# Kernel optimization log

Measured on AMD Instinct MI355X. Metric: run time of the kernel, lower is better.

The kernel has to match this reference:

```python
import jax, jax.numpy as jnp
import numpy as np

CH, G, K, STRIDE, RR = 256, 16, 7, 1, 4
GROUP = CH // G            # channels per group
PAD = (K - 1) // 2
BN_EPS = 1e-5


def setup_inputs() -> dict:
    key = jax.random.key(0)
    ks = jax.random.split(key, 9)
    b, dim = 16, 4096
    hid = CH // RR  # 64
    return {
        "x": jax.random.normal(ks[0], (b, CH, dim), jnp.float32),
        "w1": jax.random.normal(ks[1], (hid, CH), jnp.float32) * (1.0 / np.sqrt(CH)),
        "b1": jax.random.normal(ks[2], (hid,), jnp.float32) * 0.02,
        "bn_gamma": 1.0 + 0.1 * jax.random.normal(ks[3], (hid,), jnp.float32),
        "bn_beta": 0.1 * jax.random.normal(ks[4], (hid,), jnp.float32),
        "bn_mean": 0.1 * jax.random.normal(ks[5], (hid,), jnp.float32),
        "bn_var": jax.random.uniform(ks[6], (hid,), jnp.float32) + 0.5,
        "w2": jax.random.normal(ks[7], (K * G, hid), jnp.float32) * (1.0 / np.sqrt(hid)),
        "b2": jax.random.normal(ks[8], (K * G,), jnp.float32) * 0.02,
    }


def _involution(x, w1, b1, bn_gamma, bn_beta, bn_mean, bn_var, w2, b2):
    b, ch, dim = x.shape
    L = dim // STRIDE  # out_dim
    # unfold: pad then gather K shifted strided views -> [b, ch, K, L]
    xp = jnp.pad(x, ((0, 0), (0, 0), (PAD, PAD)))
    unfolded = jnp.stack(
        [xp[:, :, k : k + STRIDE * (L - 1) + 1 : STRIDE] for k in range(K)], axis=2
    )
    unfolded = unfolded.reshape(b, G, GROUP, K, L)
    # adaptive max pool to L (windows of size STRIDE); identity when STRIDE == 1
    pooled = x.reshape(b, ch, L, STRIDE).max(axis=-1)
    # kernel generator: 1x1 conv -> relu -> batchnorm (inference) -> 1x1 conv
    h = jnp.einsum("oc,bcl->bol", w1, pooled) + b1[:, None]
    h = jax.nn.relu(h)
    h = (h - bn_mean[:, None]) * jax.lax.rsqrt(bn_var[:, None] + BN_EPS)
    h = h * bn_gamma[:, None] + bn_beta[:, None]
    kern = jnp.einsum("oc,bcl->bol", w2, h) + b2[:, None]  # [b, K*G, L]
    kern = kern.reshape(b, G, K, L)
    # per-location dynamic kernel multiply + reduce over K
    out = jnp.einsum("bgkl,bgckl->bgcl", kern, unfolded)
    return out.reshape(b, ch, L)


def reference(x, w1, b1, bn_gamma, bn_beta, bn_mean, bn_var, w2, b2):
    return _involution(x, w1, b1, bn_gamma, bn_beta, bn_mean, bn_var, w2, b2)
```

## Files before the change

kernel.cpp:

```cpp
#include <hip/hip_runtime.h>

#define BB   16
#define CHN  256
#define DIMN 4096
#define KK   7
#define PADK 3
#define HID  64
#define KGN  112
#define TLC  64
#define NPAN 8
#define PCH  32
#define XSTD 33
#define HSTH 70
#define KSTD 66
#define BN_EPS 1e-5f

typedef __fp16 half2_t __attribute__((ext_vector_type(2)));
typedef __fp16 half8   __attribute__((ext_vector_type(8)));
typedef float  f32x4   __attribute__((ext_vector_type(4)));

union U32H2 { unsigned int u; half2_t h; };

static __device__ __forceinline__ unsigned int packf(float a, float b) {
    U32H2 t; t.h = __builtin_amdgcn_cvt_pkrtz(a, b); return t.u;
}
static __device__ __forceinline__ half2_t ash2(unsigned int u) { U32H2 t; t.u = u; return t.h; }
static __device__ __forceinline__ __fp16 u16h(unsigned short u) {
    return __builtin_bit_cast(__fp16, u);
}
static __device__ __forceinline__ unsigned short hu16(__fp16 h) {
    return __builtin_bit_cast(unsigned short, h);
}

__global__ __launch_bounds__(256) void setup_k(
    const float* __restrict__ w1, const float* __restrict__ w2,
    const float* __restrict__ bn_gamma, const float* __restrict__ bn_beta,
    const float* __restrict__ bn_mean,  const float* __restrict__ bn_var,
    __fp16* __restrict__ w1f, __fp16* __restrict__ w2f,
    float* __restrict__ scb, float* __restrict__ shb) {
    int t = blockIdx.x * 256 + threadIdx.x;
    if (t < HID * CHN) w1f[t] = (__fp16)w1[t];
    if (t < KGN * HID) w2f[t] = (__fp16)w2[t];
    if (t < HID) {
        float s = bn_gamma[t] * rsqrtf(bn_var[t] + BN_EPS);
        scb[t] = s;
        shb[t] = bn_beta[t] - bn_mean[t] * s;
    }
}

template <int OFF>
static __device__ __forceinline__ void extract_kv(const uint4 q[4], float kv[KK][4]) {
#pragma unroll
    for (int k = 0; k < KK; ++k) {
        const int kk = k + OFF;
        const int i  = kk >> 1;
        const int h  = kk & 1;
#pragma unroll
        for (int j = 0; j < 4; ++j) {
            unsigned int u = (&q[i].x)[j];
            half2_t hh = ash2(u);
            kv[k][j] = h ? (float)hh[1] : (float)hh[0];
        }
    }
}

__global__ __launch_bounds__(256, 4) void fused_k(
    const float* __restrict__ x,
    const __fp16* __restrict__ w1f,
    const float* __restrict__ b1,
    const float* __restrict__ scb, const float* __restrict__ shb,
    const __fp16* __restrict__ w2f,
    const float* __restrict__ b2,
    float* __restrict__ out) {
    __shared__ unsigned int   xs[2][PCH * XSTD];
    __shared__ unsigned short hs[HID * HSTH];
    __shared__ unsigned int   ks[56 * KSTD];

    const int t    = threadIdx.x;
    const int lane = t & 63;
    const int w    = t >> 6;
    const int lr   = t & 15;
    const int lg   = (t >> 4) & 3;
    const int b    = blockIdx.x >> 6;
    const int l0   = (blockIdx.x & 63) * TLC;
    const int colL = 16 * w + lr;

    const unsigned short* xs16[2] = {
        (const unsigned short*)xs[0], (const unsigned short*)xs[1] };

    const int colq = t & 15;
    const int chl  = t >> 4;
    const float* xg = x + ((size_t)b * CHN + chl) * DIMN + l0 + 4 * colq;

    float4 pre[2];
#pragma unroll
    for (int i = 0; i < 2; ++i)
        pre[i] = *(const float4*)(xg + (size_t)(16 * i) * DIMN);
#pragma unroll
    for (int i = 0; i < 2; ++i) {
        uint2 v;
        v.x = packf(pre[i].x, pre[i].y);
        v.y = packf(pre[i].z, pre[i].w);
        *(uint2*)&xs[0][(chl + 16 * i) * XSTD + 2 * colq] = v;
    }
    __syncthreads();

    f32x4 acc[4];
#pragma unroll
    for (int of = 0; of < 4; ++of) acc[of] = (f32x4){0.f, 0.f, 0.f, 0.f};

    for (int p = 0; p < NPAN; ++p) {
        if (p + 1 < NPAN) {
#pragma unroll
            for (int i = 0; i < 2; ++i)
                pre[i] = *(const float4*)(xg + (size_t)(32 * (p + 1) + 16 * i) * DIMN);
        }
        const unsigned short* xb = xs16[p & 1];
        half8 bf;
#pragma unroll
        for (int j = 0; j < 8; ++j)
            bf[j] = u16h(xb[(8 * lg + j) * (2 * XSTD) + colL]);
#pragma unroll
        for (int of = 0; of < 4; ++of) {
            half8 af = *(const half8*)(w1f + (16 * of + lr) * CHN + PCH * p + 8 * lg);
            acc[of] = __builtin_amdgcn_mfma_f32_16x16x32_f16(af, bf, acc[of], 0, 0, 0);
        }
        if (p + 1 < NPAN) {
            __syncthreads();
#pragma unroll
            for (int i = 0; i < 2; ++i) {
                uint2 v;
                v.x = packf(pre[i].x, pre[i].y);
                v.y = packf(pre[i].z, pre[i].w);
                *(uint2*)&xs[(p + 1) & 1][(chl + 16 * i) * XSTD + 2 * colq] = v;
            }
            __syncthreads();
        }
    }

#pragma unroll
    for (int of = 0; of < 4; ++of) {
#pragma unroll
        for (int r = 0; r < 4; ++r) {
            const int o = 16 * of + 4 * lg + r;
            float hv = fmaxf(acc[of][r] + b1[o], 0.f) * scb[o] + shb[o];
            hs[o * HSTH + colL] = hu16((__fp16)hv);
        }
    }

    f32x4 acc2[7];
#pragma unroll
    for (int rf = 0; rf < 7; ++rf) acc2[rf] = (f32x4){0.f, 0.f, 0.f, 0.f};

#pragma unroll
    for (int kx = 0; kx < 2; ++kx) {
        half8 bf;
#pragma unroll
        for (int j = 0; j < 8; ++j)
            bf[j] = u16h(hs[(32 * kx + 8 * lg + j) * HSTH + colL]);
#pragma unroll
        for (int rf = 0; rf < 7; ++rf) {
            half8 af = *(const half8*)(w2f + (16 * rf + lr) * HID + 32 * kx + 8 * lg);
            acc2[rf] = __builtin_amdgcn_mfma_f32_16x16x32_f16(af, bf, acc2[rf], 0, 0, 0);
        }
    }

#pragma unroll
    for (int rf = 0; rf < 7; ++rf) {
#pragma unroll
        for (int p = 0; p < 2; ++p) {
            const int r0 = 16 * rf + 4 * lg + 2 * p;
            float k0 = acc2[rf][2 * p + 0] + b2[r0 + 0];
            float k1 = acc2[rf][2 * p + 1] + b2[r0 + 1];
            ks[(r0 >> 1) * KSTD + colL] = packf(k0, k1);
        }
    }
    __syncthreads();

    const int q4   = lane & 15;
    const int hi   = lane >> 4;
    const int col0 = l0 + 4 * q4;

#pragma unroll
    for (int gi = 0; gi < 4; ++gi) {
        const int g   = 4 * w + gi;
        const int rpb = (7 * g) >> 1;
        uint4 qq[4];
#pragma unroll
        for (int ii = 0; ii < 4; ++ii)
            qq[ii] = *(const uint4*)(ks + (rpb + ii) * KSTD + 4 * q4);
        float kv[KK][4];
        if ((gi & 1) == 0) extract_kv<0>(qq, kv);
        else               extract_kv<1>(qq, kv);

#pragma unroll 4
        for (int i2 = 0; i2 < 4; ++i2) {
            const int ch = 16 * g + 4 * i2 + hi;
            const float* xrow = x + ((size_t)b * CHN + ch) * DIMN;
            float4 fa = *(const float4*)(xrow + (col0 > 0 ? col0 - 4 : 0));
            float4 fb = *(const float4*)(xrow + col0);
            float4 fc = *(const float4*)(xrow + (col0 + 4 < DIMN ? col0 + 4 : DIMN - 4));

            float xr[10] = { fa.y, fa.z, fa.w, fb.x, fb.y, fb.z, fb.w, fc.x, fc.y, fc.z };
            if (col0 == 0)        { xr[0] = 0.f; xr[1] = 0.f; xr[2] = 0.f; }
            if (col0 == DIMN - 4) { xr[7] = 0.f; xr[8] = 0.f; xr[9] = 0.f; }

            float o0 = 0.f, o1 = 0.f, o2 = 0.f, o3 = 0.f;
#pragma unroll
            for (int k = 0; k < KK; ++k) {
                o0 = fmaf(kv[k][0], xr[k + 0], o0);
                o1 = fmaf(kv[k][1], xr[k + 1], o1);
                o2 = fmaf(kv[k][2], xr[k + 2], o2);
                o3 = fmaf(kv[k][3], xr[k + 3], o3);
            }
            *(float4*)(out + ((size_t)b * CHN + ch) * DIMN + col0) =
                make_float4(o0, o1, o2, o3);
        }
    }
}

extern "C" void kernel_launch(void* const* d_in, const int* in_sizes, int n_in,
                              void* d_out, int out_size, void* d_ws, size_t ws_size,
                              hipStream_t stream) {
    (void)in_sizes; (void)n_in; (void)out_size; (void)ws_size;

    const float* x        = (const float*)d_in[0];
    const float* w1       = (const float*)d_in[1];
    const float* b1       = (const float*)d_in[2];
    const float* bn_gamma = (const float*)d_in[3];
    const float* bn_beta  = (const float*)d_in[4];
    const float* bn_mean  = (const float*)d_in[5];
    const float* bn_var   = (const float*)d_in[6];
    const float* w2       = (const float*)d_in[7];
    const float* b2       = (const float*)d_in[8];
    float*       out      = (float*)d_out;

    __fp16* w1f = (__fp16*)d_ws;
    __fp16* w2f = w1f + HID * CHN;
    float*  scb = (float*)(w2f + KGN * HID);
    float*  shb = scb + HID;

    setup_k<<<(HID * CHN + 255) / 256, 256, 0, stream>>>(
        w1, w2, bn_gamma, bn_beta, bn_mean, bn_var, w1f, w2f, scb, shb);
    fused_k<<<BB * (DIMN / TLC), 256, 0, stream>>>(
        x, w1f, b1, scb, shb, w2f, b2, out);
}
```

Before: 61.00 us.

## Stage whole fp16 x tile with halo in LDS and reuse for involution

Loads all 256 channels of the 64-column x tile, plus 3-element halos on each side, into LDS as fp16 in a single pass. This replaces the double-buffered per-panel pipeline. The involution stage then reads x from LDS instead of re-reading it from global memory, which removes the second global read of x. The trade-offs are that the involution now uses fp16-rounded x values, which costs precision, and that LDS use grows to about 50KB, so occupancy is lowered to 3 blocks. The hs and ks buffers now share one LDS region, which needs an extra barrier.

```diff
diff --git a/kernel.cpp b/kernel.cpp
--- a/kernel.cpp
+++ b/kernel.cpp
@@ -8,11 +8,10 @@
 #define HID  64
 #define KGN  112
 #define TLC  64
-#define NPAN 8
-#define PCH  32
-#define XSTD 33
+#define XSD  35
+#define XSH  70
 #define HSTH 70
-#define KSTD 66
+#define KSTD 68
 #define BN_EPS 1e-5f
 
 typedef __fp16 half2_t __attribute__((ext_vector_type(2)));
@@ -64,7 +63,7 @@
     }
 }
 
-__global__ __launch_bounds__(256, 4) void fused_k(
+__global__ __launch_bounds__(256, 3) void fused_k(
     const float* __restrict__ x,
     const __fp16* __restrict__ w1f,
     const float* __restrict__ b1,
@@ -72,9 +71,12 @@
     const __fp16* __restrict__ w2f,
     const float* __restrict__ b2,
     float* __restrict__ out) {
-    __shared__ unsigned int   xs[2][PCH * XSTD];
-    __shared__ unsigned short hs[HID * HSTH];
-    __shared__ unsigned int   ks[56 * KSTD];
+    __shared__ unsigned int xs[CHN * XSD];
+    __shared__ unsigned int un[56 * KSTD];
+
+    unsigned short* xs16 = (unsigned short*)xs;
+    unsigned short* hs16 = (unsigned short*)un;
+    unsigned int*   ks   = un;
 
     const int t    = threadIdx.x;
     const int lane = t & 63;
@@ -85,23 +87,33 @@
     const int l0   = (blockIdx.x & 63) * TLC;
     const int colL = 16 * w + lr;
 
-    const unsigned short* xs16[2] = {
-        (const unsigned short*)xs[0], (const unsigned short*)xs[1] };
-
-    const int colq = t & 15;
-    const int chl  = t >> 4;
-    const float* xg = x + ((size_t)b * CHN + chl) * DIMN + l0 + 4 * colq;
-
-    float4 pre[2];
-#pragma unroll
-    for (int i = 0; i < 2; ++i)
-        pre[i] = *(const float4*)(xg + (size_t)(16 * i) * DIMN);
-#pragma unroll
-    for (int i = 0; i < 2; ++i) {
-        uint2 v;
-        v.x = packf(pre[i].x, pre[i].y);
-        v.y = packf(pre[i].z, pre[i].w);
-        *(uint2*)&xs[0][(chl + 16 * i) * XSTD + 2 * colq] = v;
+    {
+        const int colq = t & 15;
+        const int chl  = t >> 4;
+        const float* xg = x + ((size_t)b * CHN + chl) * DIMN + l0 + 4 * colq;
+        float4 v[16];
+#pragma unroll
+        for (int i = 0; i < 16; ++i)
+            v[i] = *(const float4*)(xg + (size_t)(16 * i) * DIMN);
+#pragma unroll
+        for (int i = 0; i < 16; ++i) {
+            unsigned short* rp = xs16 + (chl + 16 * i) * XSH + 4 * colq + 3;
+            rp[0] = hu16((__fp16)v[i].x);
+            *(unsigned int*)(rp + 1) = packf(v[i].y, v[i].z);
+            rp[3] = hu16((__fp16)v[i].w);
+        }
+        const float* xrow = x + ((size_t)b * CHN + t) * DIMN;
+        float4 lv = (l0 > 0) ? *(const float4*)(xrow + l0 - 4)
+                             : make_float4(0.f, 0.f, 0.f, 0.f);
+        float4 rv = (l0 + TLC < DIMN) ? *(const float4*)(xrow + l0 + TLC)
+                                      : make_float4(0.f, 0.f, 0.f, 0.f);
+        unsigned short* hp = xs16 + t * XSH;
+        hp[0]  = hu16((__fp16)lv.y);
+        hp[1]  = hu16((__fp16)lv.z);
+        hp[2]  = hu16((__fp16)lv.w);
+        hp[67] = hu16((__fp16)rv.x);
+        hp[68] = hu16((__fp16)rv.y);
+        hp[69] = hu16((__fp16)rv.z);
     }
     __syncthreads();
 
@@ -109,32 +121,16 @@
 #pragma unroll
     for (int of = 0; of < 4; ++of) acc[of] = (f32x4){0.f, 0.f, 0.f, 0.f};
 
-    for (int p = 0; p < NPAN; ++p) {
-        if (p + 1 < NPAN) {
-#pragma unroll
-            for (int i = 0; i < 2; ++i)
-                pre[i] = *(const float4*)(xg + (size_t)(32 * (p + 1) + 16 * i) * DIMN);
-        }
-        const unsigned short* xb = xs16[p & 1];
+#pragma unroll
+    for (int p = 0; p < 8; ++p) {
         half8 bf;
 #pragma unroll
         for (int j = 0; j < 8; ++j)
-            bf[j] = u16h(xb[(8 * lg + j) * (2 * XSTD) + colL]);
+            bf[j] = u16h(xs16[(32 * p + 8 * lg + j) * XSH + colL + 3]);
 #pragma unroll
         for (int of = 0; of < 4; ++of) {
-            half8 af = *(const half8*)(w1f + (16 * of + lr) * CHN + PCH * p + 8 * lg);
+            half8 af = *(const half8*)(w1f + (16 * of + lr) * CHN + 32 * p + 8 * lg);
             acc[of] = __builtin_amdgcn_mfma_f32_16x16x32_f16(af, bf, acc[of], 0, 0, 0);
-        }
-        if (p + 1 < NPAN) {
-            __syncthreads();
-#pragma unroll
-            for (int i = 0; i < 2; ++i) {
-                uint2 v;
-                v.x = packf(pre[i].x, pre[i].y);
-                v.y = packf(pre[i].z, pre[i].w);
-                *(uint2*)&xs[(p + 1) & 1][(chl + 16 * i) * XSTD + 2 * colq] = v;
-            }
-            __syncthreads();
         }
     }
 
@@ -144,7 +140,7 @@
         for (int r = 0; r < 4; ++r) {
             const int o = 16 * of + 4 * lg + r;
             float hv = fmaxf(acc[of][r] + b1[o], 0.f) * scb[o] + shb[o];
-            hs[o * HSTH + colL] = hu16((__fp16)hv);
+            hs16[o * HSTH + colL] = hu16((__fp16)hv);
         }
     }
 
@@ -157,13 +153,15 @@
         half8 bf;
 #pragma unroll
         for (int j = 0; j < 8; ++j)
-            bf[j] = u16h(hs[(32 * kx + 8 * lg + j) * HSTH + colL]);
+            bf[j] = u16h(hs16[(32 * kx + 8 * lg + j) * HSTH + colL]);
 #pragma unroll
         for (int rf = 0; rf < 7; ++rf) {
             half8 af = *(const half8*)(w2f + (16 * rf + lr) * HID + 32 * kx + 8 * lg);
             acc2[rf] = __builtin_amdgcn_mfma_f32_16x16x32_f16(af, bf, acc2[rf], 0, 0, 0);
         }
     }
+
+    __syncthreads();
 
 #pragma unroll
     for (int rf = 0; rf < 7; ++rf) {
@@ -177,9 +175,9 @@
     }
     __syncthreads();
 
-    const int q4   = lane & 15;
-    const int hi   = lane >> 4;
-    const int col0 = l0 + 4 * q4;
+    const int q4    = lane & 15;
+    const int hi    = lane >> 4;
+    const int cbase = 4 * q4;
 
 #pragma unroll
     for (int gi = 0; gi < 4; ++gi) {
@@ -188,32 +186,33 @@
         uint4 qq[4];
 #pragma unroll
         for (int ii = 0; ii < 4; ++ii)
-            qq[ii] = *(const uint4*)(ks + (rpb + ii) * KSTD + 4 * q4);
+            qq[ii] = *(const uint4*)(ks + (rpb + ii) * KSTD + cbase);
         float kv[KK][4];
-        if ((gi & 1) == 0) extract_kv<0>(qq, kv);
-        else               extract_kv<1>(qq, kv);
-
-#pragma unroll 4
+        if ((g & 1) == 0) extract_kv<0>(qq, kv);
+        else              extract_kv<1>(qq, kv);
+
+#pragma unroll
         for (int i2 = 0; i2 < 4; ++i2) {
             const int ch = 16 * g + 4 * i2 + hi;
-            const float* xrow = x + ((size_t)b * CHN + ch) * DIMN;
-            float4 fa = *(const float4*)(xrow + (col0 > 0 ? col0 - 4 : 0));
-            float4 fb = *(const float4*)(xrow + col0);
-            float4 fc = *(const float4*)(xrow + (col0 + 4 < DIMN ? col0 + 4 : DIMN - 4));
-
-            float xr[10] = { fa.y, fa.z, fa.w, fb.x, fb.y, fb.z, fb.w, fc.x, fc.y, fc.z };
-            if (col0 == 0)        { xr[0] = 0.f; xr[1] = 0.f; xr[2] = 0.f; }
-            if (col0 == DIMN - 4) { xr[7] = 0.f; xr[8] = 0.f; xr[9] = 0.f; }
-
+            const unsigned int* xr = xs + ch * XSD + (cbase >> 1);
+            unsigned int uu[5];
+#pragma unroll
+            for (int j = 0; j < 5; ++j) uu[j] = xr[j];
+            float xv[10];
+#pragma unroll
+            for (int r = 0; r < 10; ++r) {
+                half2_t hh = ash2(uu[r >> 1]);
+                xv[r] = (r & 1) ? (float)hh[1] : (float)hh[0];
+            }
             float o0 = 0.f, o1 = 0.f, o2 = 0.f, o3 = 0.f;
 #pragma unroll
             for (int k = 0; k < KK; ++k) {
-                o0 = fmaf(kv[k][0], xr[k + 0], o0);
-                o1 = fmaf(kv[k][1], xr[k + 1], o1);
-                o2 = fmaf(kv[k][2], xr[k + 2], o2);
-                o3 = fmaf(kv[k][3], xr[k + 3], o3);
+                o0 = fmaf(kv[k][0], xv[k + 0], o0);
+                o1 = fmaf(kv[k][1], xv[k + 1], o1);
+                o2 = fmaf(kv[k][2], xv[k + 2], o2);
+                o3 = fmaf(kv[k][3], xv[k + 3], o3);
             }
-            *(float4*)(out + ((size_t)b * CHN + ch) * DIMN + col0) =
+            *(float4*)(out + ((size_t)b * CHN + ch) * DIMN + l0 + cbase) =
                 make_float4(o0, o1, o2, o3);
         }
     }
```

New measurement: 55.90 us. 8.4% less time.

## Enlarge column tile to 256 and reuse w1/w2 fragments across column fragments

Applied to the files above, without the earlier changes.

Each block now covers 256 columns instead of 64, so there are 256 blocks instead of 1024. Each wave computes four column fragments in the first GEMM and two per pass in the second, reusing the weight fragments loaded from global memory. The x staging panels alias the kernel-weight LDS region to fit the larger tile, and the output stage processes one channel per lane with contiguous 256-column rows. In exchange, occupancy drops to one block per CU with heavy register pressure, and with 256 blocks on the GPU's CUs latency hiding may suffer.

```diff
diff --git a/kernel.cpp b/kernel.cpp
--- a/kernel.cpp
+++ b/kernel.cpp
@@ -4,15 +4,15 @@
 #define CHN  256
 #define DIMN 4096
 #define KK   7
-#define PADK 3
 #define HID  64
 #define KGN  112
-#define TLC  64
+#define TLC  256
 #define NPAN 8
 #define PCH  32
-#define XSTD 33
-#define HSTH 70
-#define KSTD 66
+#define PSTD 131
+#define KSTD 260
+#define HS_DW (HID * PSTD)
+#define KS_DW (56 * KSTD)
 #define BN_EPS 1e-5f
 
 typedef __fp16 half2_t __attribute__((ext_vector_type(2)));
@@ -27,9 +27,6 @@
 static __device__ __forceinline__ half2_t ash2(unsigned int u) { U32H2 t; t.u = u; return t.h; }
 static __device__ __forceinline__ __fp16 u16h(unsigned short u) {
     return __builtin_bit_cast(__fp16, u);
-}
-static __device__ __forceinline__ unsigned short hu16(__fp16 h) {
-    return __builtin_bit_cast(unsigned short, h);
 }
 
 __global__ __launch_bounds__(256) void setup_k(
@@ -64,7 +61,7 @@
     }
 }
 
-__global__ __launch_bounds__(256, 4) void fused_k(
+__global__ __launch_bounds__(256, 1) void fused_k(
     const float* __restrict__ x,
     const __fp16* __restrict__ w1f,
     const float* __restrict__ b1,
@@ -72,114 +69,136 @@
     const __fp16* __restrict__ w2f,
     const float* __restrict__ b2,
     float* __restrict__ out) {
-    __shared__ unsigned int   xs[2][PCH * XSTD];
-    __shared__ unsigned short hs[HID * HSTH];
-    __shared__ unsigned int   ks[56 * KSTD];
+    __shared__ unsigned int lds[HS_DW + KS_DW];
+    unsigned short* hs16 = (unsigned short*)lds;
+    unsigned int*   ks   = lds + HS_DW;
+    unsigned int*   pan0 = ks;
+    unsigned int*   pan1 = ks + PCH * PSTD;
 
     const int t    = threadIdx.x;
     const int lane = t & 63;
     const int w    = t >> 6;
     const int lr   = t & 15;
     const int lg   = (t >> 4) & 3;
-    const int b    = blockIdx.x >> 6;
-    const int l0   = (blockIdx.x & 63) * TLC;
-    const int colL = 16 * w + lr;
-
-    const unsigned short* xs16[2] = {
-        (const unsigned short*)xs[0], (const unsigned short*)xs[1] };
-
-    const int colq = t & 15;
-    const int chl  = t >> 4;
-    const float* xg = x + ((size_t)b * CHN + chl) * DIMN + l0 + 4 * colq;
-
-    float4 pre[2];
-#pragma unroll
-    for (int i = 0; i < 2; ++i)
-        pre[i] = *(const float4*)(xg + (size_t)(16 * i) * DIMN);
-#pragma unroll
-    for (int i = 0; i < 2; ++i) {
-        uint2 v;
-        v.x = packf(pre[i].x, pre[i].y);
-        v.y = packf(pre[i].z, pre[i].w);
-        *(uint2*)&xs[0][(chl + 16 * i) * XSTD + 2 * colq] = v;
+    const int b    = blockIdx.x >> 4;
+    const int l0   = (blockIdx.x & 15) * TLC;
+
+    const int cq  = t & 63;
+    const int rr0 = t >> 6;
+    const float* xg = x + (size_t)b * CHN * DIMN + l0 + 4 * cq;
+
+    float4 v[8];
+#pragma unroll
+    for (int i = 0; i < 8; ++i)
+        v[i] = *(const float4*)(xg + (size_t)(rr0 + 4 * i) * DIMN);
+#pragma unroll
+    for (int i = 0; i < 8; ++i) {
+        uint2 u;
+        u.x = packf(v[i].x, v[i].y);
+        u.y = packf(v[i].z, v[i].w);
+        *(uint2*)&pan0[(rr0 + 4 * i) * PSTD + 2 * cq] = u;
     }
     __syncthreads();
 
-    f32x4 acc[4];
-#pragma unroll
-    for (int of = 0; of < 4; ++of) acc[of] = (f32x4){0.f, 0.f, 0.f, 0.f};
+    f32x4 acc[4][4];
+#pragma unroll
+    for (int of = 0; of < 4; ++of)
+#pragma unroll
+        for (int cf = 0; cf < 4; ++cf) acc[of][cf] = (f32x4){0.f, 0.f, 0.f, 0.f};
 
     for (int p = 0; p < NPAN; ++p) {
         if (p + 1 < NPAN) {
 #pragma unroll
-            for (int i = 0; i < 2; ++i)
-                pre[i] = *(const float4*)(xg + (size_t)(32 * (p + 1) + 16 * i) * DIMN);
-        }
-        const unsigned short* xb = xs16[p & 1];
-        half8 bf;
-#pragma unroll
-        for (int j = 0; j < 8; ++j)
-            bf[j] = u16h(xb[(8 * lg + j) * (2 * XSTD) + colL]);
-#pragma unroll
-        for (int of = 0; of < 4; ++of) {
-            half8 af = *(const half8*)(w1f + (16 * of + lr) * CHN + PCH * p + 8 * lg);
-            acc[of] = __builtin_amdgcn_mfma_f32_16x16x32_f16(af, bf, acc[of], 0, 0, 0);
+            for (int i = 0; i < 8; ++i)
+                v[i] = *(const float4*)(xg + (size_t)(32 * (p + 1) + rr0 + 4 * i) * DIMN);
+        }
+        const unsigned short* pb = (const unsigned short*)((p & 1) ? pan1 : pan0);
+        half8 af[4];
+#pragma unroll
+        for (int of = 0; of < 4; ++of)
+            af[of] = *(const half8*)(w1f + (16 * of + lr) * CHN + 32 * p + 8 * lg);
+#pragma unroll
+        for (int cf = 0; cf < 4; ++cf) {
+            half8 bf;
+#pragma unroll
+            for (int j = 0; j < 8; ++j)
+                bf[j] = u16h(pb[(8 * lg + j) * (2 * PSTD) + 64 * w + 16 * cf + lr]);
+#pragma unroll
+            for (int of = 0; of < 4; ++of)
+                acc[of][cf] = __builtin_amdgcn_mfma_f32_16x16x32_f16(af[of], bf, acc[of][cf], 0, 0, 0);
         }
         if (p + 1 < NPAN) {
             __syncthreads();
-#pragma unroll
-            for (int i = 0; i < 2; ++i) {
-                uint2 v;
-                v.x = packf(pre[i].x, pre[i].y);
-                v.y = packf(pre[i].z, pre[i].w);
-                *(uint2*)&xs[(p + 1) & 1][(chl + 16 * i) * XSTD + 2 * colq] = v;
+            unsigned int* pw = ((p + 1) & 1) ? pan1 : pan0;
+#pragma unroll
+            for (int i = 0; i < 8; ++i) {
+                uint2 u;
+                u.x = packf(v[i].x, v[i].y);
+                u.y = packf(v[i].z, v[i].w);
+                *(uint2*)&pw[(rr0 + 4 * i) * PSTD + 2 * cq] = u;
             }
             __syncthreads();
         }
     }
-
-#pragma unroll
-    for (int of = 0; of < 4; ++of) {
+    __syncthreads();
+
+#pragma unroll
+    for (int of = 0; of < 4; ++of)
 #pragma unroll
         for (int r = 0; r < 4; ++r) {
-            const int o = 16 * of + 4 * lg + r;
-            float hv = fmaxf(acc[of][r] + b1[o], 0.f) * scb[o] + shb[o];
-            hs[o * HSTH + colL] = hu16((__fp16)hv);
-        }
-    }
-
-    f32x4 acc2[7];
-#pragma unroll
-    for (int rf = 0; rf < 7; ++rf) acc2[rf] = (f32x4){0.f, 0.f, 0.f, 0.f};
-
-#pragma unroll
-    for (int kx = 0; kx < 2; ++kx) {
-        half8 bf;
-#pragma unroll
-        for (int j = 0; j < 8; ++j)
-            bf[j] = u16h(hs[(32 * kx + 8 * lg + j) * HSTH + colL]);
-#pragma unroll
-        for (int rf = 0; rf < 7; ++rf) {
-            half8 af = *(const half8*)(w2f + (16 * rf + lr) * HID + 32 * kx + 8 * lg);
-            acc2[rf] = __builtin_amdgcn_mfma_f32_16x16x32_f16(af, bf, acc2[rf], 0, 0, 0);
-        }
-    }
-
-#pragma unroll
-    for (int rf = 0; rf < 7; ++rf) {
-#pragma unroll
-        for (int p = 0; p < 2; ++p) {
-            const int r0 = 16 * rf + 4 * lg + 2 * p;
-            float k0 = acc2[rf][2 * p + 0] + b2[r0 + 0];
-            float k1 = acc2[rf][2 * p + 1] + b2[r0 + 1];
-            ks[(r0 >> 1) * KSTD + colL] = packf(k0, k1);
-        }
+            const int o  = 16 * of + 4 * lg + r;
+            const float bo = b1[o], sc = scb[o], sh = shb[o];
+#pragma unroll
+            for (int cf = 0; cf < 4; ++cf) {
+                float hv = fmaxf(acc[of][cf][r] + bo, 0.f) * sc + sh;
+                hs16[o * (2 * PSTD) + 64 * w + 16 * cf + lr] =
+                    __builtin_bit_cast(unsigned short, (__fp16)hv);
+            }
+        }
+
+#pragma unroll
+    for (int ch2 = 0; ch2 < 2; ++ch2) {
+        f32x4 acc2[7][2];
+#pragma unroll
+        for (int rf = 0; rf < 7; ++rf)
+#pragma unroll
+            for (int cc = 0; cc < 2; ++cc) acc2[rf][cc] = (f32x4){0.f, 0.f, 0.f, 0.f};
+
+#pragma unroll
+        for (int kx = 0; kx < 2; ++kx) {
+            half8 bf[2];
+#pragma unroll
+            for (int cc = 0; cc < 2; ++cc) {
+                const int col = 64 * w + 16 * (2 * ch2 + cc) + lr;
+#pragma unroll
+                for (int j = 0; j < 8; ++j)
+                    bf[cc][j] = u16h(hs16[(32 * kx + 8 * lg + j) * (2 * PSTD) + col]);
+            }
+#pragma unroll
+            for (int rf = 0; rf < 7; ++rf) {
+                half8 af2 = *(const half8*)(w2f + (16 * rf + lr) * HID + 32 * kx + 8 * lg);
+                acc2[rf][0] = __builtin_amdgcn_mfma_f32_16x16x32_f16(af2, bf[0], acc2[rf][0], 0, 0, 0);
+                acc2[rf][1] = __builtin_amdgcn_mfma_f32_16x16x32_f16(af2, bf[1], acc2[rf][1], 0, 0, 0);
+            }
+        }
+#pragma unroll
+        for (int rf = 0; rf < 7; ++rf)
+#pragma unroll
+            for (int p2 = 0; p2 < 2; ++p2) {
+                const int r0 = 16 * rf + 4 * lg + 2 * p2;
+                const float ba = b2[r0], bb2 = b2[r0 + 1];
+#pragma unroll
+                for (int cc = 0; cc < 2; ++cc) {
+                    const int col = 64 * w + 16 * (2 * ch2 + cc) + lr;
+                    ks[(r0 >> 1) * KSTD + col] =
+                        packf(acc2[rf][cc][2 * p2 + 0] + ba, acc2[rf][cc][2 * p2 + 1] + bb2);
+                }
+            }
     }
     __syncthreads();
 
-    const int q4   = lane & 15;
-    const int hi   = lane >> 4;
-    const int col0 = l0 + 4 * q4;
+    const int cb   = 4 * lane;
+    const int col0 = l0 + cb;
 
 #pragma unroll
     for (int gi = 0; gi < 4; ++gi) {
@@ -188,22 +207,22 @@
         uint4 qq[4];
 #pragma unroll
         for (int ii = 0; ii < 4; ++ii)
-            qq[ii] = *(const uint4*)(ks + (rpb + ii) * KSTD + 4 * q4);
+            qq[ii] = *(const uint4*)(ks + (rpb + ii) * KSTD + cb);
         float kv[KK][4];
         if ((gi & 1) == 0) extract_kv<0>(qq, kv);
         else               extract_kv<1>(qq, kv);
 
 #pragma unroll 4
-        for (int i2 = 0; i2 < 4; ++i2) {
-            const int ch = 16 * g + 4 * i2 + hi;
+        for (int i2 = 0; i2 < 16; ++i2) {
+            const int ch = 16 * g + i2;
             const float* xrow = x + ((size_t)b * CHN + ch) * DIMN;
-            float4 fa = *(const float4*)(xrow + (col0 > 0 ? col0 - 4 : 0));
+            float4 fa = (col0 > 0) ? *(const float4*)(xrow + col0 - 4)
+                                   : make_float4(0.f, 0.f, 0.f, 0.f);
             float4 fb = *(const float4*)(xrow + col0);
-            float4 fc = *(const float4*)(xrow + (col0 + 4 < DIMN ? col0 + 4 : DIMN - 4));
+            float4 fc = (col0 + 4 < DIMN) ? *(const float4*)(xrow + col0 + 4)
+                                          : make_float4(0.f, 0.f, 0.f, 0.f);
 
             float xr[10] = { fa.y, fa.z, fa.w, fb.x, fb.y, fb.z, fb.w, fc.x, fc.y, fc.z };
-            if (col0 == 0)        { xr[0] = 0.f; xr[1] = 0.f; xr[2] = 0.f; }
-            if (col0 == DIMN - 4) { xr[7] = 0.f; xr[8] = 0.f; xr[9] = 0.f; }
 
             float o0 = 0.f, o1 = 0.f, o2 = 0.f, o3 = 0.f;
 #pragma unroll
```

Result: slower. 66.37 us (+8.8%).
